# Optimization experiments

Hardware: AMD Instinct MI355X
Metric: run time of the kernel (lower is better)

Reference implementation:

```python
import jax, jax.numpy as jnp
import numpy as np

VOCAB, EMBED, HID = 50257, 512, 512
B, SRC = 128, 128


def setup_inputs() -> dict:
    key = jax.random.key(0)
    ks = jax.random.split(key, 16)
    s = 0.02
    emb_tab = jax.random.normal(ks[0], (VOCAB, EMBED), jnp.float32) * s
    emb_tab = emb_tab.at[0].set(0.0)  # padding_idx=0
    return {
        "x": jax.random.randint(ks[1], (B,), 0, VOCAB),
        "decoder_hidden": jax.random.normal(ks[2], (1, B, HID), jnp.float32),
        "source_lens": jax.random.randint(ks[3], (B,), 1, SRC + 1),
        "encoder_outputs": jax.random.normal(ks[4], (B, SRC, HID), jnp.float32),
        "context_vec": jax.random.normal(ks[5], (B, HID), jnp.float32),
        "embedding": emb_tab,
        "w_ih": jax.random.normal(ks[6], (3 * HID, HID + EMBED), jnp.float32) * s,
        "w_hh": jax.random.normal(ks[7], (3 * HID, HID), jnp.float32) * s,
        "b_ih": jax.random.normal(ks[8], (3 * HID,), jnp.float32) * s,
        "b_hh": jax.random.normal(ks[9], (3 * HID,), jnp.float32) * s,
        "Wa": jax.random.normal(ks[10], (HID, HID), jnp.float32) * s,
        "Wc": jax.random.normal(ks[11], (HID, 2 * HID), jnp.float32) * s,
        "fc1_w": jax.random.normal(ks[12], (VOCAB, HID), jnp.float32) * s,
        "fc1_b": jax.random.normal(ks[13], (VOCAB,), jnp.float32) * s,
    }


def _gru_step(inp, h, w_ih, w_hh, b_ih, b_hh):
    # inp: [B, I], h: [B, H] -> h': [B, H]  (PyTorch GRU gate order: r, z, n)
    gi = inp @ w_ih.T + b_ih
    gh = h @ w_hh.T + b_hh
    i_r, i_z, i_n = jnp.split(gi, 3, axis=1)
    h_r, h_z, h_n = jnp.split(gh, 3, axis=1)
    r = jax.nn.sigmoid(i_r + h_r)
    z = jax.nn.sigmoid(i_z + h_z)
    n = jnp.tanh(i_n + r * h_n)
    return (1.0 - z) * n + z * h


def reference(x, decoder_hidden, source_lens, encoder_outputs, context_vec,
              embedding, w_ih, w_hh, b_ih, b_hh, Wa, Wc, fc1_w, fc1_b):
    # embedding lookup (dropout is identity in eval mode)
    emb = embedding[x]                                    # [B, E]
    rnn_in = jnp.concatenate([emb, context_vec], axis=1)  # [B, E+H]
    h = _gru_step(rnn_in, decoder_hidden[0], w_ih, w_hh, b_ih, b_hh)  # [B, H]
    hidden = h[None]                                      # [1, B, H]

    # Luong-style attention (scores laid out [src_len, B] as in original)
    q = h @ Wa.T                                          # [B, H]
    attn_scores = jnp.einsum('bsh,bh->sb', encoder_outputs, q)  # [S, B]
    seq_range = jnp.arange(encoder_outputs.shape[1])      # [S]
    enc_mask = (seq_range[None, :] < source_lens[:, None]).T    # [S, B]
    masked = enc_mask.astype(attn_scores.dtype) * attn_scores
    masked = jnp.where(masked == 0, jnp.asarray(-1e10, masked.dtype), masked)
    a = jax.nn.softmax(masked, axis=0)                    # [S, B]
    ctx = jnp.einsum('sb,bsh->bh', a, encoder_outputs)    # [B, H]
    ctx = jnp.tanh(jnp.concatenate([ctx, h], axis=1) @ Wc.T)    # [B, H]

    logits = ctx @ fc1_w.T + fc1_b                        # [B, V]
    log_probs = jax.nn.log_softmax(logits, axis=1)
    return log_probs, hidden, a, ctx
```

## Files before the change

### kernel.cpp

```cpp
#include <hip/hip_runtime.h>

#define VOCAB 50257
#define EMBED 512
#define HID   512
#define B     128
#define SRC   128
#define FBLK2 3142

typedef __attribute__((ext_vector_type(8))) short short8;
typedef __attribute__((ext_vector_type(4))) float f32x4;

__device__ __forceinline__ unsigned f2bf(float x) {
    unsigned u = __builtin_bit_cast(unsigned, x);
    return (u + 0x7fffu + ((u >> 16) & 1u)) >> 16;
}
__device__ __forceinline__ unsigned pk2(float lo, float hi) {
    return f2bf(lo) | (f2bf(hi) << 16);
}
__device__ __forceinline__ uint4 pk8(const float* p) {
    uint4 r;
    r.x = pk2(p[0], p[1]); r.y = pk2(p[2], p[3]);
    r.z = pk2(p[4], p[5]); r.w = pk2(p[6], p[7]);
    return r;
}
__device__ __forceinline__ uint4 pk8v(float4 a, float4 b) {
    uint4 r;
    r.x = pk2(a.x, a.y); r.y = pk2(a.z, a.w);
    r.z = pk2(b.x, b.y); r.w = pk2(b.z, b.w);
    return r;
}


__global__ void k_embed_pack(const int* __restrict__ x, const float* __restrict__ ctxv,
                             const float* __restrict__ emb, const float* __restrict__ h0,
                             uint4* __restrict__ apk_rnn, uint4* __restrict__ apk_h0) {
    __shared__ float buf[1024];
    __shared__ float hbuf[512];
    const int b = blockIdx.x, t = threadIdx.x;
    const int row = x[b];
    if (t < 128) {
        ((float4*)buf)[t]  = ((const float4*)(emb + (size_t)row * EMBED))[t];
        ((float4*)hbuf)[t] = ((const float4*)(h0 + (size_t)b * HID))[t];
    } else {
        ((float4*)buf)[t] = ((const float4*)(ctxv + (size_t)b * HID))[t - 128];
    }
    __syncthreads();
    const int mt = b >> 4, lb = b & 15;
    if (t < 128) {
        int kc = t >> 4, ksl = (t >> 2) & 3, kg = t & 3;
        apk_rnn[((kc * 8 + mt) * 4 + ksl) * 64 + kg * 16 + lb] = pk8(&buf[t * 8]);
    } else if (t < 192) {
        int i = t - 128;
        int kc = i >> 4, ksl = (i >> 2) & 3, kg = i & 3;
        apk_h0[((kc * 8 + mt) * 4 + ksl) * 64 + kg * 16 + lb] = pk8(&hbuf[i * 8]);
    }
}

__global__ __launch_bounds__(256, 2) void k_gemm2(
        const uint4* __restrict__ apkA, const float* __restrict__ WA,
        const float* __restrict__ bA, float* __restrict__ CA, int KA,
        const uint4* __restrict__ apkB, const float* __restrict__ WB,
        const float* __restrict__ bB, float* __restrict__ CB, int KB,
        int nblkA) {
    const bool isB = (int)blockIdx.x >= nblkA;
    const uint4* apk = isB ? apkB : apkA;
    const float* W   = isB ? WB : WA;
    const float* bias= isB ? bB : bA;
    float* C         = isB ? CB : CA;
    const int K      = isB ? KB : KA;
    const int bid    = isB ? (int)blockIdx.x - nblkA : (int)blockIdx.x;
    const int N = 1536;
    __shared__ float red[4][128][16];
    const int tid = threadIdx.x, lane = tid & 63, wv = tid >> 6;
    const int n0 = bid * 16;
    const int ncol = n0 + (lane & 15);
    const int kg = lane >> 4;
    const int spw = K >> 7;
    f32x4 acc[8];
#pragma unroll
    for (int mt = 0; mt < 8; ++mt) acc[mt] = (f32x4)0.f;
    const float4* W4 = (const float4*)W;
    const size_t wb = (size_t)ncol * (K >> 2) + kg * 2;
    for (int s = 0; s < spw; ++s) {
        const int ks = wv * spw + s;
        float4 w0 = W4[wb + ks * 8];
        float4 w1 = W4[wb + ks * 8 + 1];
        short8 bf = __builtin_bit_cast(short8, pk8v(w0, w1));
        const uint4* ap = apk + ((size_t)(ks >> 2) * 32 + (ks & 3)) * 64 + lane;
#pragma unroll
        for (int mt = 0; mt < 8; ++mt) {
            short8 af = __builtin_bit_cast(short8, ap[mt * 256]);
            acc[mt] = __builtin_amdgcn_mfma_f32_16x16x32_bf16(af, bf, acc[mt], 0, 0, 0);
        }
    }
#pragma unroll
    for (int mt = 0; mt < 8; ++mt)
#pragma unroll
        for (int j = 0; j < 4; ++j)
            red[wv][mt * 16 + kg * 4 + j][lane & 15] = acc[mt][j];
    __syncthreads();
#pragma unroll
    for (int i = 0; i < 8; ++i) {
        int o = tid + i * 256;
        int r = o >> 4, c = o & 15;
        float v = red[0][r][c] + red[1][r][c] + red[2][r][c] + red[3][r][c];
        v += bias[n0 + c];
        C[(size_t)r * N + n0 + c] = v;
    }
}

template <int N, int K, int ACT, int HASB, int PACK>
__global__ __launch_bounds__(256, 2) void k_gemm_ks(
        const uint4* __restrict__ apk, const float* __restrict__ W,
        const float* __restrict__ bias, float* __restrict__ C,
        uint4* __restrict__ apk_out) {
    __shared__ float red[4][128][16];
    const int tid = threadIdx.x, lane = tid & 63, wv = tid >> 6;
    const int n0 = blockIdx.x * 16;
    const int ncol = n0 + (lane & 15);
    const int nc = ncol < N ? ncol : N - 1;
    const int kg = lane >> 4;
    constexpr int SPW = K / 128;
    f32x4 acc[8];
#pragma unroll
    for (int mt = 0; mt < 8; ++mt) acc[mt] = (f32x4)0.f;
    const float4* W4 = (const float4*)W;
    const size_t wb = (size_t)nc * (K / 4) + kg * 2;
#pragma unroll
    for (int s = 0; s < SPW; ++s) {
        const int ks = wv * SPW + s;
        float4 w0 = W4[wb + ks * 8];
        float4 w1 = W4[wb + ks * 8 + 1];
        short8 bf = __builtin_bit_cast(short8, pk8v(w0, w1));
        const uint4* ap = apk + (((ks >> 2) * 8) * 4 + (ks & 3)) * 64 + lane;
#pragma unroll
        for (int mt = 0; mt < 8; ++mt) {
            short8 af = __builtin_bit_cast(short8, ap[mt * 256]);
            acc[mt] = __builtin_amdgcn_mfma_f32_16x16x32_bf16(af, bf, acc[mt], 0, 0, 0);
        }
    }
#pragma unroll
    for (int mt = 0; mt < 8; ++mt)
#pragma unroll
        for (int j = 0; j < 4; ++j)
            red[wv][mt * 16 + kg * 4 + j][lane & 15] = acc[mt][j];
    __syncthreads();
#pragma unroll
    for (int i = 0; i < 8; ++i) {
        int o = tid + i * 256;
        int r = o >> 4, c = o & 15;
        float v = red[0][r][c] + red[1][r][c] + red[2][r][c] + red[3][r][c];
        if (HASB) v += bias[n0 + c];
        if (ACT) v = tanhf(v);
        C[(size_t)r * N + n0 + c] = v;
        if (PACK) red[0][r][c] = v;
    }
    if constexpr (PACK) {
        __syncthreads();
        int r = tid >> 1, hf = tid & 1;
        float tmp[8];
#pragma unroll
        for (int z = 0; z < 8; ++z) tmp[z] = red[0][r][hf * 8 + z];
        int k0 = n0 + hf * 8;
        int kc = k0 >> 7, ksl = (k0 >> 5) & 3, kg2 = (k0 >> 3) & 3;
        apk_out[((kc * 8 + (r >> 4)) * 4 + ksl) * 64 + kg2 * 16 + (r & 15)] = pk8(tmp);
    }
}

__global__ void k_gru(const float* __restrict__ gi, const float* __restrict__ gh,
                      const float* __restrict__ h0, float* __restrict__ h,
                      uint4* __restrict__ apk_h) {
    __shared__ float hsh[256];
    const int t = threadIdx.x;
    const int idx = blockIdx.x * 256 + t;
    const int b = blockIdx.x >> 1, half = blockIdx.x & 1;
    const int j = half * 256 + t;
    const float* gib = gi + (size_t)b * 1536;
    const float* ghb = gh + (size_t)b * 1536;
    float ir = gib[j], iz = gib[512 + j], inn = gib[1024 + j];
    float hr = ghb[j], hz = ghb[512 + j], hn = ghb[1024 + j];
    float r = 1.f / (1.f + expf(-(ir + hr)));
    float z = 1.f / (1.f + expf(-(iz + hz)));
    float nn = tanhf(inn + r * hn);
    float hv = (1.f - z) * nn + z * h0[idx];
    h[idx] = hv;
    hsh[t] = hv;
    __syncthreads();
    if (t < 32) {
        int k0 = half * 256 + t * 8;
        int kc = k0 >> 7, ksl = (k0 >> 5) & 3, kg = (k0 >> 3) & 3;
        apk_h[((kc * 8 + (b >> 4)) * 4 + ksl) * 64 + kg * 16 + (b & 15)] = pk8(&hsh[t * 8]);
    }
}

__global__ __launch_bounds__(512) void k_attn(const float* __restrict__ enc,
        const float* __restrict__ q, const int* __restrict__ lens,
        const float* __restrict__ h, float* __restrict__ a_out,
        uint4* __restrict__ apk_cat) {
    __shared__ float qs[512];
    __shared__ float red[128];
    __shared__ float aw[128];
    __shared__ float catsh[1024];
    const int b = blockIdx.x, t = threadIdx.x;
    qs[t] = q[(size_t)b * 512 + t];
    __syncthreads();
    const int srow = t >> 2, part = t & 3;
    const float* ep = enc + ((size_t)b * SRC + srow) * 512 + part * 128;
    float s = 0.f;
#pragma unroll
    for (int k4 = 0; k4 < 32; ++k4) {
        float4 e = ((const float4*)ep)[k4];
        float4 qq = *(const float4*)&qs[part * 128 + k4 * 4];
        s = fmaf(e.x, qq.x, fmaf(e.y, qq.y, fmaf(e.z, qq.z, fmaf(e.w, qq.w, s))));
    }
    s += __shfl_xor(s, 1);
    s += __shfl_xor(s, 2);
    if (part == 0) {
        int len = lens[b];
        float val = (srow < len) ? s : 0.f;
        if (val == 0.f) val = -1e10f;
        red[srow] = val;
        aw[srow] = val;
    }
    __syncthreads();
    for (int off = 64; off > 0; off >>= 1) {
        if (t < off) red[t] = fmaxf(red[t], red[t + off]);
        __syncthreads();
    }
    float mx = red[0];
    __syncthreads();
    if (t < 128) { float e = expf(aw[t] - mx); aw[t] = e; red[t] = e; }
    __syncthreads();
    for (int off = 64; off > 0; off >>= 1) {
        if (t < off) red[t] += red[t + off];
        __syncthreads();
    }
    float denom = red[0];
    if (t < 128) {
        float av = aw[t] / denom;
        aw[t] = av;
        a_out[(size_t)t * B + b] = av;
    }
    __syncthreads();
    float a0 = 0.f;
    const float* e2 = enc + (size_t)b * (SRC * 512) + t;
#pragma unroll 4
    for (int s2 = 0; s2 < SRC; ++s2) a0 = fmaf(aw[s2], e2[(size_t)s2 * 512], a0);
    catsh[t] = a0;
    catsh[512 + t] = h[(size_t)b * 512 + t];
    __syncthreads();
    if (t < 128) {
        int kc = t >> 4, ksl = (t >> 2) & 3, kg = t & 3;
        apk_cat[((kc * 8 + (b >> 4)) * 4 + ksl) * 64 + kg * 16 + (b & 15)] =
            pk8(&catsh[t * 8]);
    }
}

__global__ __launch_bounds__(64, 2) void k_fc1e(
        const uint4* __restrict__ apk, const float* __restrict__ W,
        const float* __restrict__ bias, float* __restrict__ C,
        float2* __restrict__ pout, int nblk) {
    const int lane = threadIdx.x;
    const int kg = lane >> 4;
    const int c0 = blockIdx.x * 16 + (lane & 15);
    const int nc0 = c0 < VOCAB ? c0 : VOCAB - 1;
    const float4* W4 = (const float4*)W;
    const size_t wb = (size_t)nc0 * 128 + kg * 2;

    float4 wf[32];
#pragma unroll
    for (int ks = 0; ks < 16; ++ks) {
        wf[2 * ks]     = W4[wb + ks * 8];
        wf[2 * ks + 1] = W4[wb + ks * 8 + 1];
    }
    f32x4 acc[8];
#pragma unroll
    for (int mt = 0; mt < 8; ++mt) acc[mt] = (f32x4)0.f;
#pragma unroll
    for (int ks = 0; ks < 16; ++ks) {
        short8 bf = __builtin_bit_cast(short8, pk8v(wf[2 * ks], wf[2 * ks + 1]));
        const uint4* ap = apk + ((size_t)(ks >> 2) * 32 + (ks & 3)) * 64 + lane;
#pragma unroll
        for (int mt = 0; mt < 8; ++mt) {
            short8 af = __builtin_bit_cast(short8, ap[mt * 256]);
            acc[mt] = __builtin_amdgcn_mfma_f32_16x16x32_bf16(af, bf, acc[mt], 0, 0, 0);
        }
    }
    const float bb = bias[nc0];
#pragma unroll
    for (int mt = 0; mt < 8; ++mt) {
#pragma unroll
        for (int j = 0; j < 4; ++j) {
            const int row = mt * 16 + kg * 4 + j;
            float v = acc[mt][j] + bb;
            if (c0 < VOCAB) C[(size_t)row * VOCAB + c0] = v;
            if (pout) {
                float va = c0 < VOCAB ? v : -1e30f;
                float m = va;
                m = fmaxf(m, __shfl_xor(m, 1));
                m = fmaxf(m, __shfl_xor(m, 2));
                m = fmaxf(m, __shfl_xor(m, 4));
                m = fmaxf(m, __shfl_xor(m, 8));
                float e = c0 < VOCAB ? __expf(va - m) : 0.f;
                e += __shfl_xor(e, 1);
                e += __shfl_xor(e, 2);
                e += __shfl_xor(e, 4);
                e += __shfl_xor(e, 8);
                if ((lane & 15) == 0)
                    pout[(size_t)row * nblk + blockIdx.x] = make_float2(m, e);
            }
        }
    }
}

__global__ __launch_bounds__(1024) void k_lse_fuse(float* __restrict__ logits,
        const float2* __restrict__ pout, int nblk) {
    const int b = blockIdx.x, t = threadIdx.x;
    float m = -1e30f, s = 0.f;
    for (int i = t; i < nblk; i += 1024) {
        float2 p = pout[(size_t)b * nblk + i];
        float mm = fmaxf(m, p.x);
        s = s * __expf(m - mm) + p.y * __expf(p.x - mm);
        m = mm;
    }
    __shared__ float sm[1024], ss[1024];
    sm[t] = m; ss[t] = s;
    __syncthreads();
    for (int off = 512; off > 0; off >>= 1) {
        if (t < off) {
            float m2 = sm[t + off], s2 = ss[t + off];
            float mm = fmaxf(sm[t], m2);
            ss[t] = ss[t] * __expf(sm[t] - mm) + s2 * __expf(m2 - mm);
            sm[t] = mm;
        }
        __syncthreads();
    }
    __shared__ float Lsh;
    if (t == 0) Lsh = sm[0] + logf(ss[0]);
    __syncthreads();
    const float L = Lsh;
    float* row = logits + (size_t)b * VOCAB;
    const int N4 = VOCAB >> 2;
    for (int i = t; i < N4; i += 1024) {
        float4 x = ((const float4*)row)[i];
        x.x -= L; x.y -= L; x.z -= L; x.w -= L;
        ((float4*)row)[i] = x;
    }
    if (t == 0) row[VOCAB - 1] -= L;
}

__global__ __launch_bounds__(1024) void k_lse_sub(float* __restrict__ logits) {
    const int b = blockIdx.x, t = threadIdx.x;
    float* row = logits + (size_t)b * VOCAB;
    const int N4 = VOCAB >> 2;
    float m = -1e30f, s = 0.f;
    for (int i = t; i < N4; i += 1024) {
        float4 x = ((const float4*)row)[i];
        float xs[4] = {x.x, x.y, x.z, x.w};
#pragma unroll
        for (int j = 0; j < 4; ++j) {
            float v = xs[j];
            if (v > m) { s = s * __expf(m - v) + 1.f; m = v; }
            else        s += __expf(v - m);
        }
    }
    if (t == 0) {
        float v = row[VOCAB - 1];
        if (v > m) { s = s * __expf(m - v) + 1.f; m = v; }
        else        s += __expf(v - m);
    }
    __shared__ float sm[1024], ss[1024];
    sm[t] = m; ss[t] = s;
    __syncthreads();
    for (int off = 512; off > 0; off >>= 1) {
        if (t < off) {
            float m2 = sm[t + off], s2 = ss[t + off];
            float mm = fmaxf(sm[t], m2);
            ss[t] = ss[t] * __expf(sm[t] - mm) + s2 * __expf(m2 - mm);
            sm[t] = mm;
        }
        __syncthreads();
    }
    __shared__ float Lsh;
    if (t == 0) Lsh = sm[0] + logf(ss[0]);
    __syncthreads();
    float L = Lsh;
    for (int i = t; i < N4; i += 1024) {
        float4 x = ((const float4*)row)[i];
        x.x -= L; x.y -= L; x.z -= L; x.w -= L;
        ((float4*)row)[i] = x;
    }
    if (t == 0) row[VOCAB - 1] -= L;
}

extern "C" void kernel_launch(void* const* d_in, const int* in_sizes, int n_in,
                              void* d_out, int out_size, void* d_ws, size_t ws_size,
                              hipStream_t stream) {
    const int*   x    = (const int*)d_in[0];
    const float* h0   = (const float*)d_in[1];
    const int*   lens = (const int*)d_in[2];
    const float* enc  = (const float*)d_in[3];
    const float* ctxv = (const float*)d_in[4];
    const float* emb  = (const float*)d_in[5];
    const float* wih  = (const float*)d_in[6];
    const float* whh  = (const float*)d_in[7];
    const float* bih  = (const float*)d_in[8];
    const float* bhh  = (const float*)d_in[9];
    const float* Wa   = (const float*)d_in[10];
    const float* Wc   = (const float*)d_in[11];
    const float* fc1w = (const float*)d_in[12];
    const float* fc1b = (const float*)d_in[13];

    float* out     = (float*)d_out;
    float* outLogp = out;
    float* outHid  = out + (size_t)B * VOCAB;
    float* outA    = outHid + (size_t)B * HID;
    float* outCtx  = outA + (size_t)SRC * B;

    float* gi = outLogp;
    float* gh = gi + B * 1536;
    float* q  = gh + B * 1536;
    uint4* apk_rnn = (uint4*)(q + B * HID);
    uint4* apk_h0  = apk_rnn + 16384;
    uint4* apk_h   = apk_h0 + 8192;
    uint4* apk_cat = apk_h + 8192;

    uint4*  apk_ctx = (uint4*)d_ws;
    size_t  off_pout = 131072;
    size_t  off_L    = off_pout + (size_t)B * FBLK2 * sizeof(float2);
    bool bigws = ws_size >= off_L + 512;
    float2* pout = bigws ? (float2*)((char*)d_ws + off_pout) : nullptr;

    k_embed_pack<<<dim3(B), dim3(256), 0, stream>>>(x, ctxv, emb, h0, apk_rnn, apk_h0);
    k_gemm2<<<dim3(192), dim3(256), 0, stream>>>(
        apk_rnn, wih, bih, gi, 1024,
        apk_h0, whh, bhh, gh, 512, 96);
    k_gru<<<dim3(256), dim3(256), 0, stream>>>(gi, gh, h0, outHid, apk_h);
    k_gemm_ks<512, 512, 0, 0, 0><<<dim3(32), dim3(256), 0, stream>>>(
        apk_h, Wa, nullptr, q, nullptr);
    k_attn<<<dim3(B), dim3(512), 0, stream>>>(enc, q, lens, outHid, outA, apk_cat);
    k_gemm_ks<512, 1024, 1, 0, 1><<<dim3(32), dim3(256), 0, stream>>>(
        apk_cat, Wc, nullptr, outCtx, apk_ctx);
    k_fc1e<<<dim3(FBLK2), dim3(64), 0, stream>>>(apk_ctx, fc1w, fc1b, outLogp,
                                                 pout, FBLK2);
    if (bigws) {
        k_lse_fuse<<<dim3(B), dim3(1024), 0, stream>>>(outLogp, pout, FBLK2);
    } else {
        k_lse_sub<<<dim3(B), dim3(1024), 0, stream>>>(outLogp);
    }
}
```

Baseline: 113.3 us.

## Share fc1 activation tiles across four waves via LDS staging

Replaces the single-wave fc1 kernel with 256-thread blocks that cover 64 vocab columns. Each block stages the packed bf16 activation chunks into LDS with global_load_lds, so four waves share them instead of each wave re-reading the whole activation matrix from L2. The K loop is split into four chunks, each followed by a barrier, and the fc1 weights are loaded one chunk at a time rather than all up front. This cuts redundant L2 traffic but may reduce how many memory loads are in flight. The partial-LSE buffer width is padded to match the new block count.

Measured after the change: 110.8 us. -2.2%, faster.

```diff
diff --git a/kernel.cpp b/kernel.cpp
--- a/kernel.cpp
+++ b/kernel.cpp
@@ -5,7 +5,8 @@
 #define HID   512
 #define B     128
 #define SRC   128
-#define FBLK2 3142
+#define FBLKC 786
+#define PW    3144
 
 typedef __attribute__((ext_vector_type(8))) short short8;
 typedef __attribute__((ext_vector_type(4))) float f32x4;
@@ -28,6 +29,11 @@
     r.x = pk2(a.x, a.y); r.y = pk2(a.z, a.w);
     r.z = pk2(b.x, b.y); r.w = pk2(b.z, b.w);
     return r;
+}
+__device__ __forceinline__ void gll16(const void* g, void* l) {
+    __builtin_amdgcn_global_load_lds(
+        (const __attribute__((address_space(1))) void*)g,
+        (__attribute__((address_space(3))) void*)l, 16, 0, 0);
 }
 
 
@@ -256,58 +262,66 @@
     }
 }
 
-__global__ __launch_bounds__(64, 2) void k_fc1e(
+__global__ __launch_bounds__(256, 4) void k_fc1c(
         const uint4* __restrict__ apk, const float* __restrict__ W,
         const float* __restrict__ bias, float* __restrict__ C,
-        float2* __restrict__ pout, int nblk) {
-    const int lane = threadIdx.x;
+        float2* __restrict__ pout) {
+    __shared__ uint4 As[2048];
+    const int tid = threadIdx.x, lane = tid & 63, wv = tid >> 6;
+    const int ncol = blockIdx.x * 64 + wv * 16 + (lane & 15);
+    const int nc = ncol < VOCAB ? ncol : VOCAB - 1;
+    const bool valid = ncol < VOCAB;
     const int kg = lane >> 4;
-    const int c0 = blockIdx.x * 16 + (lane & 15);
-    const int nc0 = c0 < VOCAB ? c0 : VOCAB - 1;
-    const float4* W4 = (const float4*)W;
-    const size_t wb = (size_t)nc0 * 128 + kg * 2;
-
-    float4 wf[32];
-#pragma unroll
-    for (int ks = 0; ks < 16; ++ks) {
-        wf[2 * ks]     = W4[wb + ks * 8];
-        wf[2 * ks + 1] = W4[wb + ks * 8 + 1];
-    }
     f32x4 acc[8];
 #pragma unroll
     for (int mt = 0; mt < 8; ++mt) acc[mt] = (f32x4)0.f;
-#pragma unroll
-    for (int ks = 0; ks < 16; ++ks) {
-        short8 bf = __builtin_bit_cast(short8, pk8v(wf[2 * ks], wf[2 * ks + 1]));
-        const uint4* ap = apk + ((size_t)(ks >> 2) * 32 + (ks & 3)) * 64 + lane;
-#pragma unroll
-        for (int mt = 0; mt < 8; ++mt) {
-            short8 af = __builtin_bit_cast(short8, ap[mt * 256]);
-            acc[mt] = __builtin_amdgcn_mfma_f32_16x16x32_bf16(af, bf, acc[mt], 0, 0, 0);
-        }
-    }
-    const float bb = bias[nc0];
+    const float* wb = W + (size_t)nc * 512 + kg * 8;
+#pragma unroll
+    for (int kc = 0; kc < 4; ++kc) {
+        if (kc) __syncthreads();
+#pragma unroll
+        for (int it = 0; it < 8; ++it)
+            gll16(apk + (size_t)kc * 2048 + it * 256 + wv * 64 + lane,
+                  As + it * 256 + wv * 64);
+        float4 w[8];
+#pragma unroll
+        for (int ksl = 0; ksl < 4; ++ksl) {
+            w[2 * ksl]     = *(const float4*)(wb + kc * 128 + ksl * 32);
+            w[2 * ksl + 1] = *(const float4*)(wb + kc * 128 + ksl * 32 + 4);
+        }
+        __syncthreads();
+#pragma unroll
+        for (int ksl = 0; ksl < 4; ++ksl) {
+            short8 bf = __builtin_bit_cast(short8, pk8v(w[2 * ksl], w[2 * ksl + 1]));
+#pragma unroll
+            for (int mt = 0; mt < 8; ++mt) {
+                short8 af = __builtin_bit_cast(short8, As[(mt * 4 + ksl) * 64 + lane]);
+                acc[mt] = __builtin_amdgcn_mfma_f32_16x16x32_bf16(af, bf, acc[mt], 0, 0, 0);
+            }
+        }
+    }
+    const float bb = bias[nc];
 #pragma unroll
     for (int mt = 0; mt < 8; ++mt) {
 #pragma unroll
         for (int j = 0; j < 4; ++j) {
             const int row = mt * 16 + kg * 4 + j;
             float v = acc[mt][j] + bb;
-            if (c0 < VOCAB) C[(size_t)row * VOCAB + c0] = v;
+            if (valid) C[(size_t)row * VOCAB + ncol] = v;
             if (pout) {
-                float va = c0 < VOCAB ? v : -1e30f;
+                float va = valid ? v : -1e30f;
                 float m = va;
                 m = fmaxf(m, __shfl_xor(m, 1));
                 m = fmaxf(m, __shfl_xor(m, 2));
                 m = fmaxf(m, __shfl_xor(m, 4));
                 m = fmaxf(m, __shfl_xor(m, 8));
-                float e = c0 < VOCAB ? __expf(va - m) : 0.f;
+                float e = valid ? __expf(va - m) : 0.f;
                 e += __shfl_xor(e, 1);
                 e += __shfl_xor(e, 2);
                 e += __shfl_xor(e, 4);
                 e += __shfl_xor(e, 8);
                 if ((lane & 15) == 0)
-                    pout[(size_t)row * nblk + blockIdx.x] = make_float2(m, e);
+                    pout[(size_t)row * PW + blockIdx.x * 4 + wv] = make_float2(m, e);
             }
         }
     }
@@ -427,7 +441,7 @@
 
     uint4*  apk_ctx = (uint4*)d_ws;
     size_t  off_pout = 131072;
-    size_t  off_L    = off_pout + (size_t)B * FBLK2 * sizeof(float2);
+    size_t  off_L    = off_pout + (size_t)B * PW * sizeof(float2);
     bool bigws = ws_size >= off_L + 512;
     float2* pout = bigws ? (float2*)((char*)d_ws + off_pout) : nullptr;
 
@@ -441,10 +455,9 @@
     k_attn<<<dim3(B), dim3(512), 0, stream>>>(enc, q, lens, outHid, outA, apk_cat);
     k_gemm_ks<512, 1024, 1, 0, 1><<<dim3(32), dim3(256), 0, stream>>>(
         apk_cat, Wc, nullptr, outCtx, apk_ctx);
-    k_fc1e<<<dim3(FBLK2), dim3(64), 0, stream>>>(apk_ctx, fc1w, fc1b, outLogp,
-                                                 pout, FBLK2);
+    k_fc1c<<<dim3(FBLKC), dim3(256), 0, stream>>>(apk_ctx, fc1w, fc1b, outLogp, pout);
     if (bigws) {
-        k_lse_fuse<<<dim3(B), dim3(1024), 0, stream>>>(outLogp, pout, FBLK2);
+        k_lse_fuse<<<dim3(B), dim3(1024), 0, stream>>>(outLogp, pout, PW);
     } else {
         k_lse_sub<<<dim3(B), dim3(1024), 0, stream>>>(outLogp);
     }
```
